# Optimization experiments

Measured on AMD Instinct MI355X. Metric: run time of the kernel, lower is better.

Reference implementation:

```python
import jax, jax.numpy as jnp
import numpy as np

B, N, D = 8, 4096, 1024
NC, NU = 8, 32            # core / universal experts (num_experts=16, occ_factor=1/4)
E = NC + NU               # 40 total experts
S = 2                     # slots per expert
HC, HU = 4 * D, D         # core hidden = 4*dim, occ hidden = 4*occ_factor*dim = dim
L2_EPS = 1e-6
LN_EPS = 1e-5


def l2norm(x):
    n = jnp.sqrt(jnp.sum(x * x, axis=-1, keepdims=True))
    return x * (1.0 / (n + L2_EPS))


def layernorm(x, g, b):
    mu = jnp.mean(x, axis=-1, keepdims=True)
    var = jnp.mean((x - mu) ** 2, axis=-1, keepdims=True)
    return (x - mu) / jnp.sqrt(var + LN_EPS) * g + b


def entmax15(z):
    # exact 1.5-entmax over last axis (sorted algorithm, Peters et al. 2019)
    z = z / 2.0
    z = z - jnp.max(z, axis=-1, keepdims=True)
    zs = -jnp.sort(-z, axis=-1)                      # descending
    K = z.shape[-1]
    k = jnp.arange(1, K + 1, dtype=z.dtype)
    mean = jnp.cumsum(zs, axis=-1) / k
    meansq = jnp.cumsum(zs * zs, axis=-1) / k
    ss = k * (meansq - mean * mean)
    delta = jnp.maximum((1.0 - ss) / k, 1e-12)
    tau = mean - jnp.sqrt(delta)
    support = jnp.sum((tau <= zs).astype(jnp.int32), axis=-1, keepdims=True)
    tau_star = jnp.take_along_axis(tau, support - 1, axis=-1)
    return jnp.maximum(z - tau_star, 0.0) ** 2


def setup_inputs() -> dict:
    key = jax.random.key(0)
    ks = jax.random.split(key, 8)
    return {
        "x": jax.random.normal(ks[0], (B, N, D), jnp.float32),
        "attn_weight": jax.random.uniform(ks[1], (B, 128), jnp.float32),
        "phi": jax.random.normal(ks[2], (E, S, D), jnp.float32) * 0.02,
        "key_gamma": jnp.ones((D,), jnp.float32),
        "key_beta": jnp.zeros((D,), jnp.float32),
        "query_gamma": jnp.ones((D,), jnp.float32),
        "query_beta": jnp.zeros((D,), jnp.float32),
        "ln_gamma": jnp.ones((D,), jnp.float32),
        "ln_beta": jnp.zeros((D,), jnp.float32),
        "scale0": jnp.asarray(0.5, jnp.float32),
        "scale1": jnp.asarray(0.5, jnp.float32),
        "core_w1": jax.random.normal(ks[3], (NC, D, HC), jnp.float32) * (D ** -0.5),
        "core_b1": jnp.zeros((NC, HC), jnp.float32),
        "core_w2": jax.random.normal(ks[4], (NC, HC, D), jnp.float32) * (HC ** -0.5),
        "core_b2": jnp.zeros((NC, D), jnp.float32),
        "occ_w1": jax.random.normal(ks[5], (NU, D, HU), jnp.float32) * (D ** -0.5),
        "occ_b1": jnp.zeros((NU, HU), jnp.float32),
        "occ_w2": jax.random.normal(ks[6], (NU, HU, D), jnp.float32) * (HU ** -0.5),
        "occ_b2": jnp.zeros((NU, D), jnp.float32),
    }


def _expert_mlp(s, w1, b1, w2, b2):
    # s: [b, e, s, d]; per-expert 2-layer MLP with exact GELU
    h = jax.nn.gelu(jnp.einsum('besd,edh->besh', s, w1) + b1[None, :, None, :], approximate=False)
    return jnp.einsum('besh,ehd->besd', h, w2) + b2[None, :, None, :]


def reference(x, attn_weight, phi, key_gamma, key_beta, query_gamma, query_beta,
              ln_gamma, ln_beta, scale0, scale1,
              core_w1, core_b1, core_w2, core_b2,
              occ_w1, occ_b1, occ_w2, occ_b2):
    # keys: OffsetScale then l2norm
    k = l2norm(x * key_gamma + key_beta)
    # queries: OffsetScale -> LayerNorm -> l2norm on phi
    q = layernorm(phi * query_gamma + query_beta, ln_gamma, ln_beta)
    q = l2norm(q)
    logits = jnp.einsum('bnd,esd->bnes', k, q)                      # [B,N,E,S]
    core_mask = (jnp.arange(E) < NC)[None, None, :, None]
    adjusted = jnp.where(core_mask, logits, jnp.asarray(-10000.0, logits.dtype))
    dispatch = jax.nn.softmax(adjusted / scale0, axis=2)            # softmax over experts
    combine = entmax15((adjusted / scale1).reshape(B, N, E * S))    # [B,N,E*S]
    slots = jnp.einsum('bnd,bnes->besd', x, dispatch)               # [B,E,S,D]
    core_out = _expert_mlp(slots[:, :NC], core_w1, core_b1, core_w2, core_b2)
    occ_out = _expert_mlp(slots[:, NC:], occ_w1, occ_b1, occ_w2, occ_b2)
    out = jnp.concatenate([core_out, occ_out], axis=1).reshape(B, E * S, D)
    return jnp.einsum('bsd,bns->bnd', out, combine)                 # [B,N,D]
```

## Files before the change

### kernel.cpp

```cpp
#include <hip/hip_runtime.h>
#include <hip/hip_bf16.h>

#define B_ 8
#define N_ 4096
#define D_ 1024

#define AS1 __attribute__((address_space(1)))
#define AS3 __attribute__((address_space(3)))
__device__ __forceinline__ void gld16(const float* g, float* l) {
    __builtin_amdgcn_global_load_lds((const AS1 void*)g, (AS3 void*)l, 16, 0, 0);
}

__global__ __launch_bounds__(64) void k_prep(
    const float* __restrict__ phi, const float* __restrict__ qg, const float* __restrict__ qb,
    const float* __restrict__ lng, const float* __restrict__ lnb,
    const float* __restrict__ kg, const float* __restrict__ kb,
    float* __restrict__ qk, float* __restrict__ cj, float* __restrict__ wbuf)
{
    int r = blockIdx.x;
    int lane = threadIdx.x;
    if (r == 16) {
        float cacc = 0.f;
#pragma unroll
        for (int c = 0; c < 16; ++c) {
            int i = c * 64 + lane;
            float g = kg[i], b = kb[i];
            wbuf[i] = g * g;
            wbuf[1024 + i] = 2.0f * g * b;
            cacc += b * b;
        }
#pragma unroll
        for (int m = 32; m; m >>= 1) cacc += __shfl_xor(cacc, m);
        if (lane == 0) wbuf[2048] = cacc;
        return;
    }
    const float* pr = phi + (size_t)r * D_;
    float v[16];
    float s1 = 0.f;
#pragma unroll
    for (int c = 0; c < 16; ++c) {
        int i = c * 64 + lane;
        v[c] = pr[i] * qg[i] + qb[i];
        s1 += v[c];
    }
#pragma unroll
    for (int m = 32; m; m >>= 1) s1 += __shfl_xor(s1, m);
    float mu = s1 * (1.0f / D_);
    float s2 = 0.f;
#pragma unroll
    for (int c = 0; c < 16; ++c) { float dd = v[c] - mu; s2 += dd * dd; }
#pragma unroll
    for (int m = 32; m; m >>= 1) s2 += __shfl_xor(s2, m);
    float var = s2 * (1.0f / D_);
    float inv = 1.0f / sqrtf(var + 1e-5f);
    float u[16];
    float s3 = 0.f;
#pragma unroll
    for (int c = 0; c < 16; ++c) {
        int i = c * 64 + lane;
        u[c] = (v[c] - mu) * inv * lng[i] + lnb[i];
        s3 += u[c] * u[c];
    }
#pragma unroll
    for (int m = 32; m; m >>= 1) s3 += __shfl_xor(s3, m);
    float rn = 1.0f / (sqrtf(s3) + 1e-6f);
    float cacc = 0.f;
#pragma unroll
    for (int c = 0; c < 16; ++c) {
        int i = c * 64 + lane;
        float qv = u[c] * rn;
        qk[(size_t)r * D_ + i] = qv * kg[i];
        cacc += qv * kb[i];
    }
#pragma unroll
    for (int m = 32; m; m >>= 1) cacc += __shfl_xor(cacc, m);
    if (lane == 0) cj[r] = cacc;
}

__global__ __launch_bounds__(256) void k_fused(
    const float* __restrict__ x, const float* __restrict__ qk,
    const float* __restrict__ wbuf, const float* __restrict__ cj,
    const float* __restrict__ s0p,
    float* __restrict__ lgbuf, float* __restrict__ spart)
{
    __shared__ float smem[18436];
    float* qs   = smem;
    float* wsd  = smem + 16384;
    float* red  = smem;
    float* sums = smem + 8704;
    float* disp = smem + 9792;

    int tid = threadIdx.x;
    int tok0 = blockIdx.x * 64;
    int wid = tid >> 6;
    int r0 = tid >> 4;
    int c4 = (tid & 15) * 4;

#pragma unroll
    for (int i = 0; i < 16; ++i)
        gld16(qk + (size_t)(i * 256 + tid) * 4, &qs[(i * 256 + wid * 64) * 4]);
#pragma unroll
    for (int i = 0; i < 2; ++i)
        gld16(wbuf + (size_t)(i * 256 + tid) * 4, &wsd[(i * 256 + wid * 64) * 4]);
    __syncthreads();

    float acc[4][17];
#pragma unroll
    for (int i = 0; i < 4; ++i)
#pragma unroll
        for (int v = 0; v < 17; ++v) acc[i][v] = 0.f;

#pragma unroll 2
    for (int dc = 0; dc < 16; ++dc) {
        float4 xv[4];
#pragma unroll
        for (int i = 0; i < 4; ++i)
            xv[i] = *(const float4*)(x + (size_t)(tok0 + i * 16 + r0) * D_ + dc * 64 + c4);
        float4 w2v = *(const float4*)(wsd + dc * 64 + c4);
        float4 w1v = *(const float4*)(wsd + 1024 + dc * 64 + c4);
#pragma unroll
        for (int i = 0; i < 4; ++i)
            acc[i][16] += (w2v.x * xv[i].x + w1v.x) * xv[i].x
                        + (w2v.y * xv[i].y + w1v.y) * xv[i].y
                        + (w2v.z * xv[i].z + w1v.z) * xv[i].z
                        + (w2v.w * xv[i].w + w1v.w) * xv[i].w;
        const float* qb = qs + dc * 64 + c4;
#pragma unroll
        for (int j = 0; j < 16; ++j) {
            float4 q4 = *(const float4*)(qb + j * 1024);
#pragma unroll
            for (int i = 0; i < 4; ++i)
                acc[i][j] += xv[i].x * q4.x + xv[i].y * q4.y
                           + xv[i].z * q4.z + xv[i].w * q4.w;
        }
    }
    __syncthreads();

#pragma unroll
    for (int half = 0; half < 2; ++half) {
#pragma unroll
        for (int u = 0; u < 2; ++u) {
            int i = half * 2 + u;
            int rr = u * 16 + r0;
#pragma unroll
            for (int v = 0; v < 17; ++v)
                red[(rr * 17 + v) * 16 + (tid & 15)] = acc[i][v];
        }
        __syncthreads();
#pragma unroll
        for (int it = 0; it < 3; ++it) {
            int idx = tid + it * 256;
            if (idx < 544) {
                const float4* p = (const float4*)(red + idx * 16);
                float4 a = p[0], b = p[1], cq = p[2], dq = p[3];
                float sum = (((a.x + a.y) + (a.z + a.w)) + ((b.x + b.y) + (b.z + b.w)))
                          + (((cq.x + cq.y) + (cq.z + cq.w)) + ((dq.x + dq.y) + (dq.z + dq.w)));
                int t = idx / 17, v = idx - t * 17;
                lgbuf[(size_t)(tok0 + half * 32 + t) * 20 + v] = sum;
                sums[(half * 32 + t) * 17 + v] = sum;
            }
        }
        __syncthreads();
    }

    if (tid < 64) {
        const float* sp = sums + tid * 17;
        float ss = sp[16] + wbuf[2048];
        float rn = 1.0f / (sqrtf(ss) + 1e-6f);
        float inv0 = 1.0f / s0p[0];
        float lg[16];
#pragma unroll
        for (int j = 0; j < 16; ++j) lg[j] = (sp[j] + cj[j]) * rn;
        float dsp[16];
#pragma unroll
        for (int sl = 0; sl < 2; ++sl) {
            float a[8], m = -1e30f;
#pragma unroll
            for (int ee = 0; ee < 8; ++ee) { a[ee] = lg[2 * ee + sl] * inv0; m = fmaxf(m, a[ee]); }
            float den = 0.f;
#pragma unroll
            for (int ee = 0; ee < 8; ++ee) { a[ee] = expf(a[ee] - m); den += a[ee]; }
            float r = 1.0f / den;
#pragma unroll
            for (int ee = 0; ee < 8; ++ee) dsp[2 * ee + sl] = a[ee] * r;
        }
#pragma unroll
        for (int q4i = 0; q4i < 4; ++q4i)
            *(float4*)(&disp[tid * 16 + q4i * 4]) =
                make_float4(dsp[q4i * 4 + 0], dsp[q4i * 4 + 1], dsp[q4i * 4 + 2], dsp[q4i * 4 + 3]);
    }
    __syncthreads();

    const float* xp = x + (size_t)tok0 * D_ + tid * 4;
    float4 acc2[16];
#pragma unroll
    for (int j = 0; j < 16; ++j) { acc2[j].x = 0.f; acc2[j].y = 0.f; acc2[j].z = 0.f; acc2[j].w = 0.f; }
#pragma unroll 8
    for (int n = 0; n < 64; ++n) {
        float4 xv = *(const float4*)(xp + (size_t)n * D_);
        const float4* q4 = (const float4*)(disp + n * 16);
        float4 s0 = q4[0], s1 = q4[1], s2 = q4[2], s3 = q4[3];
        acc2[0].x  += s0.x * xv.x; acc2[0].y  += s0.x * xv.y; acc2[0].z  += s0.x * xv.z; acc2[0].w  += s0.x * xv.w;
        acc2[1].x  += s0.y * xv.x; acc2[1].y  += s0.y * xv.y; acc2[1].z  += s0.y * xv.z; acc2[1].w  += s0.y * xv.w;
        acc2[2].x  += s0.z * xv.x; acc2[2].y  += s0.z * xv.y; acc2[2].z  += s0.z * xv.z; acc2[2].w  += s0.z * xv.w;
        acc2[3].x  += s0.w * xv.x; acc2[3].y  += s0.w * xv.y; acc2[3].z  += s0.w * xv.z; acc2[3].w  += s0.w * xv.w;
        acc2[4].x  += s1.x * xv.x; acc2[4].y  += s1.x * xv.y; acc2[4].z  += s1.x * xv.z; acc2[4].w  += s1.x * xv.w;
        acc2[5].x  += s1.y * xv.x; acc2[5].y  += s1.y * xv.y; acc2[5].z  += s1.y * xv.z; acc2[5].w  += s1.y * xv.w;
        acc2[6].x  += s1.z * xv.x; acc2[6].y  += s1.z * xv.y; acc2[6].z  += s1.z * xv.z; acc2[6].w  += s1.z * xv.w;
        acc2[7].x  += s1.w * xv.x; acc2[7].y  += s1.w * xv.y; acc2[7].z  += s1.w * xv.z; acc2[7].w  += s1.w * xv.w;
        acc2[8].x  += s2.x * xv.x; acc2[8].y  += s2.x * xv.y; acc2[8].z  += s2.x * xv.z; acc2[8].w  += s2.x * xv.w;
        acc2[9].x  += s2.y * xv.x; acc2[9].y  += s2.y * xv.y; acc2[9].z  += s2.y * xv.z; acc2[9].w  += s2.y * xv.w;
        acc2[10].x += s2.z * xv.x; acc2[10].y += s2.z * xv.y; acc2[10].z += s2.z * xv.z; acc2[10].w += s2.z * xv.w;
        acc2[11].x += s2.w * xv.x; acc2[11].y += s2.w * xv.y; acc2[11].z += s2.w * xv.z; acc2[11].w += s2.w * xv.w;
        acc2[12].x += s3.x * xv.x; acc2[12].y += s3.x * xv.y; acc2[12].z += s3.x * xv.z; acc2[12].w += s3.x * xv.w;
        acc2[13].x += s3.y * xv.x; acc2[13].y += s3.y * xv.y; acc2[13].z += s3.y * xv.z; acc2[13].w += s3.y * xv.w;
        acc2[14].x += s3.z * xv.x; acc2[14].y += s3.z * xv.y; acc2[14].z += s3.z * xv.z; acc2[14].w += s3.z * xv.w;
        acc2[15].x += s3.w * xv.x; acc2[15].y += s3.w * xv.y; acc2[15].z += s3.w * xv.z; acc2[15].w += s3.w * xv.w;
    }
    float* op = spart + ((size_t)blockIdx.x * 16) * 1024 + tid * 4;
#pragma unroll
    for (int j = 0; j < 16; ++j)
        *(float4*)(op + (size_t)j * 1024) = acc2[j];
}

__global__ __launch_bounds__(64) void k_epi(
    const float* __restrict__ lgbuf, const float* __restrict__ cj,
    const float* __restrict__ wbuf, const float* __restrict__ s1p,
    float* __restrict__ combine)
{
    int tok = blockIdx.x * 64 + threadIdx.x;
    const float* lp = lgbuf + (size_t)tok * 20;
    float s[17];
    float4 q0 = *(const float4*)(lp + 0);
    float4 q1 = *(const float4*)(lp + 4);
    float4 q2 = *(const float4*)(lp + 8);
    float4 q3 = *(const float4*)(lp + 12);
    s[0] = q0.x; s[1] = q0.y; s[2] = q0.z; s[3] = q0.w;
    s[4] = q1.x; s[5] = q1.y; s[6] = q1.z; s[7] = q1.w;
    s[8] = q2.x; s[9] = q2.y; s[10] = q2.z; s[11] = q2.w;
    s[12] = q3.x; s[13] = q3.y; s[14] = q3.z; s[15] = q3.w;
    s[16] = lp[16];

    float ss = s[16] + wbuf[2048];
    float rn = 1.0f / (sqrtf(ss) + 1e-6f);
    float inv1h = 0.5f / s1p[0];
    float lg[16];
#pragma unroll
    for (int j = 0; j < 16; ++j) lg[j] = (s[j] + cj[j]) * rn;

    float z[16], zmax = -1e30f;
#pragma unroll
    for (int j = 0; j < 16; ++j) { z[j] = lg[j] * inv1h; zmax = fmaxf(zmax, z[j]); }
#pragma unroll
    for (int j = 0; j < 16; ++j) z[j] -= zmax;
    float zsr[16];
#pragma unroll
    for (int j = 0; j < 16; ++j) zsr[j] = z[j];
#pragma unroll
    for (int rr = 0; rr < 16; ++rr) {
#pragma unroll
        for (int jj = (rr & 1); jj + 1 < 16; jj += 2) {
            float aa = zsr[jj], bb = zsr[jj + 1];
            zsr[jj] = fmaxf(aa, bb);
            zsr[jj + 1] = fminf(aa, bb);
        }
    }
    float cs = 0.f, css = 0.f, tau_star = 0.f;
#pragma unroll
    for (int kk = 1; kk <= 16; ++kk) {
        cs += zsr[kk - 1];
        css += zsr[kk - 1] * zsr[kk - 1];
        float fk = (float)kk;
        float mean = cs / fk, msq = css / fk;
        float ssv = fk * (msq - mean * mean);
        float delta = fmaxf((1.0f - ssv) / fk, 1e-12f);
        float tau = mean - sqrtf(delta);
        tau_star = (tau <= zsr[kk - 1]) ? tau : tau_star;
    }
    float4* cw = (float4*)(combine + (size_t)tok * 16);
#pragma unroll
    for (int q4i = 0; q4i < 4; ++q4i) {
        float4 cv;
        float t0 = fmaxf(z[q4i * 4 + 0] - tau_star, 0.f);
        float t1 = fmaxf(z[q4i * 4 + 1] - tau_star, 0.f);
        float t2 = fmaxf(z[q4i * 4 + 2] - tau_star, 0.f);
        float t3 = fmaxf(z[q4i * 4 + 3] - tau_star, 0.f);
        cv.x = t0 * t0; cv.y = t1 * t1; cv.z = t2 * t2; cv.w = t3 * t3;
        cw[q4i] = cv;
    }
}

__global__ __launch_bounds__(256) void k_slots_reduce(
    const float* __restrict__ spart, float* __restrict__ slotsT)
{
    int j = blockIdx.x, b = blockIdx.y;
    int tid = threadIdx.x;
    const float* p = spart + ((size_t)(b * 64) * 16 + j) * 1024 + tid * 4;
    float4 s; s.x = 0.f; s.y = 0.f; s.z = 0.f; s.w = 0.f;
#pragma unroll 8
    for (int nc = 0; nc < 64; ++nc) {
        float4 v = *(const float4*)(p + (size_t)nc * 16384);
        s.x += v.x; s.y += v.y; s.z += v.z; s.w += v.w;
    }
    int e = j >> 1, sl = j & 1;
    int t = b * 2 + sl;
    float* o = slotsT + ((size_t)e * 1024 + tid * 4) * 16 + t;
    o[0] = s.x; o[16] = s.y; o[32] = s.z; o[48] = s.w;
}

__global__ __launch_bounds__(256) void k_mlp1(
    const float* __restrict__ w1, const float* __restrict__ slotsT,
    float* __restrict__ p1)
{
    __shared__ float sm[1024];
    int cc = blockIdx.x, ks = blockIdx.y, e = blockIdx.z;
    int tid = threadIdx.x;
    int k0 = ks * 64;
    int col = cc * 1024 + tid * 4;
    ((float4*)sm)[tid] = ((const float4*)(slotsT + ((size_t)e * 1024 + k0) * 16))[tid];
    __syncthreads();

    const float* wp = w1 + (size_t)e * 1024 * 4096 + (size_t)k0 * 4096 + col;
    float4 acc[16];
#pragma unroll
    for (int t = 0; t < 16; ++t) { acc[t].x = 0.f; acc[t].y = 0.f; acc[t].z = 0.f; acc[t].w = 0.f; }
#pragma unroll 8
    for (int kk = 0; kk < 64; ++kk) {
        float4 w = *(const float4*)(wp + (size_t)kk * 4096);
        const float4* q4 = (const float4*)(sm + kk * 16);
        float4 s0 = q4[0], s1 = q4[1], s2 = q4[2], s3 = q4[3];
        acc[0].x  += s0.x * w.x; acc[0].y  += s0.x * w.y; acc[0].z  += s0.x * w.z; acc[0].w  += s0.x * w.w;
        acc[1].x  += s0.y * w.x; acc[1].y  += s0.y * w.y; acc[1].z  += s0.y * w.z; acc[1].w  += s0.y * w.w;
        acc[2].x  += s0.z * w.x; acc[2].y  += s0.z * w.y; acc[2].z  += s0.z * w.z; acc[2].w  += s0.z * w.w;
        acc[3].x  += s0.w * w.x; acc[3].y  += s0.w * w.y; acc[3].z  += s0.w * w.z; acc[3].w  += s0.w * w.w;
        acc[4].x  += s1.x * w.x; acc[4].y  += s1.x * w.y; acc[4].z  += s1.x * w.z; acc[4].w  += s1.x * w.w;
        acc[5].x  += s1.y * w.x; acc[5].y  += s1.y * w.y; acc[5].z  += s1.y * w.z; acc[5].w  += s1.y * w.w;
        acc[6].x  += s1.z * w.x; acc[6].y  += s1.z * w.y; acc[6].z  += s1.z * w.z; acc[6].w  += s1.z * w.w;
        acc[7].x  += s1.w * w.x; acc[7].y  += s1.w * w.y; acc[7].z  += s1.w * w.z; acc[7].w  += s1.w * w.w;
        acc[8].x  += s2.x * w.x; acc[8].y  += s2.x * w.y; acc[8].z  += s2.x * w.z; acc[8].w  += s2.x * w.w;
        acc[9].x  += s2.y * w.x; acc[9].y  += s2.y * w.y; acc[9].z  += s2.y * w.z; acc[9].w  += s2.y * w.w;
        acc[10].x += s2.z * w.x; acc[10].y += s2.z * w.y; acc[10].z += s2.z * w.z; acc[10].w += s2.z * w.w;
        acc[11].x += s2.w * w.x; acc[11].y += s2.w * w.y; acc[11].z += s2.w * w.z; acc[11].w += s2.w * w.w;
        acc[12].x += s3.x * w.x; acc[12].y += s3.x * w.y; acc[12].z += s3.x * w.z; acc[12].w += s3.x * w.w;
        acc[13].x += s3.y * w.x; acc[13].y += s3.y * w.y; acc[13].z += s3.y * w.z; acc[13].w += s3.y * w.w;
        acc[14].x += s3.z * w.x; acc[14].y += s3.z * w.y; acc[14].z += s3.z * w.z; acc[14].w += s3.z * w.w;
        acc[15].x += s3.w * w.x; acc[15].y += s3.w * w.y; acc[15].z += s3.w * w.z; acc[15].w += s3.w * w.w;
    }
    float av0[16], av1[16], av2[16], av3[16];
#pragma unroll
    for (int t = 0; t < 16; ++t) { av0[t] = acc[t].x; av1[t] = acc[t].y; av2[t] = acc[t].z; av3[t] = acc[t].w; }
    float* op = p1 + (((size_t)ks * 8 + e) * 4096 + col) * 16;
#pragma unroll
    for (int q = 0; q < 4; ++q) {
        *(float4*)(op + 0 * 16 + q * 4) = make_float4(av0[q*4+0], av0[q*4+1], av0[q*4+2], av0[q*4+3]);
        *(float4*)(op + 1 * 16 + q * 4) = make_float4(av1[q*4+0], av1[q*4+1], av1[q*4+2], av1[q*4+3]);
        *(float4*)(op + 2 * 16 + q * 4) = make_float4(av2[q*4+0], av2[q*4+1], av2[q*4+2], av2[q*4+3]);
        *(float4*)(op + 3 * 16 + q * 4) = make_float4(av3[q*4+0], av3[q*4+1], av3[q*4+2], av3[q*4+3]);
    }
}

__global__ __launch_bounds__(256) void k_mlp2f(
    const float* __restrict__ w2, const float* __restrict__ p1,
    const float* __restrict__ b1, float* __restrict__ p2)
{
    __shared__ float sm[1024];
    int ks = blockIdx.x, e = blockIdx.y;
    int tid = threadIdx.x;
    int k0 = ks * 64;
    int col = tid * 4;

    {
        int fidx = tid;
        const float* pp = p1 + (size_t)e * 65536 + (size_t)k0 * 16 + fidx * 4;
        float4 s; s.x = 0.f; s.y = 0.f; s.z = 0.f; s.w = 0.f;
#pragma unroll
        for (int ksp = 0; ksp < 16; ++ksp) {
            float4 v = *(const float4*)(pp + (size_t)ksp * 524288);
            s.x += v.x; s.y += v.y; s.z += v.z; s.w += v.w;
        }
        int colh = k0 + (fidx >> 2);
        float bb = b1[(size_t)e * 4096 + colh];
        s.x += bb; s.y += bb; s.z += bb; s.w += bb;
        s.x = 0.5f * s.x * (1.0f + erff(s.x * 0.70710678118654752f));
        s.y = 0.5f * s.y * (1.0f + erff(s.y * 0.70710678118654752f));
        s.z = 0.5f * s.z * (1.0f + erff(s.z * 0.70710678118654752f));
        s.w = 0.5f * s.w * (1.0f + erff(s.w * 0.70710678118654752f));
        *(float4*)(&sm[fidx * 4]) = s;
    }
    __syncthreads();

    const float* wp = w2 + (size_t)e * 4096 * 1024 + (size_t)k0 * 1024 + col;
    float4 acc[16];
#pragma unroll
    for (int t = 0; t < 16; ++t) { acc[t].x = 0.f; acc[t].y = 0.f; acc[t].z = 0.f; acc[t].w = 0.f; }
#pragma unroll 8
    for (int kk = 0; kk < 64; ++kk) {
        float4 w = *(const float4*)(wp + (size_t)kk * 1024);
        const float4* q4 = (const float4*)(sm + kk * 16);
        float4 s0 = q4[0], s1 = q4[1], s2 = q4[2], s3 = q4[3];
        acc[0].x  += s0.x * w.x; acc[0].y  += s0.x * w.y; acc[0].z  += s0.x * w.z; acc[0].w  += s0.x * w.w;
        acc[1].x  += s0.y * w.x; acc[1].y  += s0.y * w.y; acc[1].z  += s0.y * w.z; acc[1].w  += s0.y * w.w;
        acc[2].x  += s0.z * w.x; acc[2].y  += s0.z * w.y; acc[2].z  += s0.z * w.z; acc[2].w  += s0.z * w.w;
        acc[3].x  += s0.w * w.x; acc[3].y  += s0.w * w.y; acc[3].z  += s0.w * w.z; acc[3].w  += s0.w * w.w;
        acc[4].x  += s1.x * w.x; acc[4].y  += s1.x * w.y; acc[4].z  += s1.x * w.z; acc[4].w  += s1.x * w.w;
        acc[5].x  += s1.y * w.x; acc[5].y  += s1.y * w.y; acc[5].z  += s1.y * w.z; acc[5].w  += s1.y * w.w;
        acc[6].x  += s1.z * w.x; acc[6].y  += s1.z * w.y; acc[6].z  += s1.z * w.z; acc[6].w  += s1.z * w.w;
        acc[7].x  += s1.w * w.x; acc[7].y  += s1.w * w.y; acc[7].z  += s1.w * w.z; acc[7].w  += s1.w * w.w;
        acc[8].x  += s2.x * w.x; acc[8].y  += s2.x * w.y; acc[8].z  += s2.x * w.z; acc[8].w  += s2.x * w.w;
        acc[9].x  += s2.y * w.x; acc[9].y  += s2.y * w.y; acc[9].z  += s2.y * w.z; acc[9].w  += s2.y * w.w;
        acc[10].x += s2.z * w.x; acc[10].y += s2.z * w.y; acc[10].z += s2.z * w.z; acc[10].w += s2.z * w.w;
        acc[11].x += s2.w * w.x; acc[11].y += s2.w * w.y; acc[11].z += s2.w * w.z; acc[11].w += s2.w * w.w;
        acc[12].x += s3.x * w.x; acc[12].y += s3.x * w.y; acc[12].z += s3.x * w.z; acc[12].w += s3.x * w.w;
        acc[13].x += s3.y * w.x; acc[13].y += s3.y * w.y; acc[13].z += s3.y * w.z; acc[13].w += s3.y * w.w;
        acc[14].x += s3.z * w.x; acc[14].y += s3.z * w.y; acc[14].z += s3.z * w.z; acc[14].w += s3.z * w.w;
        acc[15].x += s3.w * w.x; acc[15].y += s3.w * w.y; acc[15].z += s3.w * w.z; acc[15].w += s3.w * w.w;
    }
    float av0[16], av1[16], av2[16], av3[16];
#pragma unroll
    for (int t = 0; t < 16; ++t) { av0[t] = acc[t].x; av1[t] = acc[t].y; av2[t] = acc[t].z; av3[t] = acc[t].w; }
    float* op = p2 + (((size_t)ks * 8 + e) * 1024 + col) * 16;
#pragma unroll
    for (int q = 0; q < 4; ++q) {
        *(float4*)(op + 0 * 16 + q * 4) = make_float4(av0[q*4+0], av0[q*4+1], av0[q*4+2], av0[q*4+3]);
        *(float4*)(op + 1 * 16 + q * 4) = make_float4(av1[q*4+0], av1[q*4+1], av1[q*4+2], av1[q*4+3]);
        *(float4*)(op + 2 * 16 + q * 4) = make_float4(av2[q*4+0], av2[q*4+1], av2[q*4+2], av2[q*4+3]);
        *(float4*)(op + 3 * 16 + q * 4) = make_float4(av3[q*4+0], av3[q*4+1], av3[q*4+2], av3[q*4+3]);
    }
}

__global__ __launch_bounds__(256) void k_red2(
    const float* __restrict__ p2, const float* __restrict__ b2,
    float* __restrict__ co)
{
    int idx = blockIdx.x * 256 + threadIdx.x;
    int q = idx & 3, d = (idx >> 2) & 1023, e = idx >> 12;
    const float* p = p2 + ((size_t)e * 1024 + d) * 16 + q * 4;
    float4 s; s.x = 0.f; s.y = 0.f; s.z = 0.f; s.w = 0.f;
#pragma unroll 8
    for (int ks = 0; ks < 64; ++ks) {
        float4 v = *(const float4*)(p + (size_t)ks * 131072);
        s.x += v.x; s.y += v.y; s.z += v.z; s.w += v.w;
    }
    float bb = b2[(size_t)e * 1024 + d];
    float vv[4] = { s.x + bb, s.y + bb, s.z + bb, s.w + bb };
#pragma unroll
    for (int u = 0; u < 4; ++u) {
        int t = q * 4 + u;
        int b = t >> 1, sl = t & 1;
        co[((size_t)b * 16 + e * 2 + sl) * 1024 + d] = vv[u];
    }
}

__global__ __launch_bounds__(256) void k_out(
    const float* __restrict__ co, const float* __restrict__ combine,
    float* __restrict__ out)
{
    __shared__ float sm[1024];
    int b = blockIdx.y, tile = blockIdx.x;
    int tid = threadIdx.x;
    ((float4*)sm)[tid] = ((const float4*)(combine + ((size_t)b * N_ + tile * 64) * 16))[tid];
    float4 cv[16];
#pragma unroll
    for (int j = 0; j < 16; ++j)
        cv[j] = ((const float4*)(co + ((size_t)b * 16 + j) * 1024))[tid];
    __syncthreads();
    float4* ob = (float4*)(out + ((size_t)b * N_ + tile * 64) * 1024) + tid;
#pragma unroll 2
    for (int it = 0; it < 64; ++it) {
        const float* cm = sm + it * 16;
        float4 acc; acc.x = 0.f; acc.y = 0.f; acc.z = 0.f; acc.w = 0.f;
#pragma unroll
        for (int j = 0; j < 16; ++j) {
            float wj = cm[j];
            acc.x += wj * cv[j].x; acc.y += wj * cv[j].y;
            acc.z += wj * cv[j].z; acc.w += wj * cv[j].w;
        }
        ob[(size_t)it * 256] = acc;
    }
}

extern "C" void kernel_launch(void* const* d_in, const int* in_sizes, int n_in,
                              void* d_out, int out_size, void* d_ws, size_t ws_size,
                              hipStream_t stream)
{
    const float* x   = (const float*)d_in[0];
    const float* phi = (const float*)d_in[2];
    const float* kg  = (const float*)d_in[3];
    const float* kb  = (const float*)d_in[4];
    const float* qg  = (const float*)d_in[5];
    const float* qb  = (const float*)d_in[6];
    const float* lng = (const float*)d_in[7];
    const float* lnb = (const float*)d_in[8];
    const float* s0  = (const float*)d_in[9];
    const float* s1  = (const float*)d_in[10];
    const float* w1  = (const float*)d_in[11];
    const float* b1  = (const float*)d_in[12];
    const float* w2  = (const float*)d_in[13];
    const float* b2  = (const float*)d_in[14];

    float* out = (float*)d_out;
    float* ws  = (float*)d_ws;

    float* qk       = ws;
    float* cj       = qk + 16384;
    float* wbuf     = cj + 16;
    float* combine  = wbuf + 2064;
    float* slotsT   = combine + 524288;
    float* co       = slotsT + 131072;
    float* lgbuf    = co + 131072;
    float* arenaA   = lgbuf + 655360;
    float* arenaB   = arenaA + 8388608;
    float* spart    = arenaA;
    float* p1       = arenaA;
    float* p2       = arenaB;

    k_prep        <<<dim3(17),        dim3(64),  0, stream>>>(phi, qg, qb, lng, lnb, kg, kb, qk, cj, wbuf);
    k_fused       <<<dim3(512),       dim3(256), 0, stream>>>(x, qk, wbuf, cj, s0, lgbuf, spart);
    k_epi         <<<dim3(512),       dim3(64),  0, stream>>>(lgbuf, cj, wbuf, s1, combine);
    k_slots_reduce<<<dim3(16, 8),     dim3(256), 0, stream>>>(spart, slotsT);
    k_mlp1        <<<dim3(4, 16, 8),  dim3(256), 0, stream>>>(w1, slotsT, p1);
    k_mlp2f       <<<dim3(64, 8),     dim3(256), 0, stream>>>(w2, p1, b1, p2);
    k_red2        <<<dim3(128),       dim3(256), 0, stream>>>(p2, b2, co);
    k_out         <<<dim3(64, 8),     dim3(256), 0, stream>>>(co, combine, out);
}
```

Measured before the change: 255.7 us.

## Double k_fused block to 512 threads, halving per-thread token work

The fused logits/dispatch kernel now runs 512 threads per block instead of 256. Each thread handles 2 tokens instead of 4 in the logits phase, and 32 tokens instead of 64 in the slot-accumulation phase, with the two halves summed through shared memory before writing spart. The w-vector staging in LDS is dropped and read directly from global memory, which shrinks shared memory. The aim is more parallelism and lower register pressure per thread, at the cost of an extra LDS reduction, more barriers, and less reuse of each q load across tokens.

```diff
diff --git a/kernel.cpp b/kernel.cpp
--- a/kernel.cpp
+++ b/kernel.cpp
@@ -77,15 +77,14 @@
     if (lane == 0) cj[r] = cacc;
 }
 
-__global__ __launch_bounds__(256) void k_fused(
+__global__ __launch_bounds__(512, 4) void k_fused(
     const float* __restrict__ x, const float* __restrict__ qk,
     const float* __restrict__ wbuf, const float* __restrict__ cj,
     const float* __restrict__ s0p,
     float* __restrict__ lgbuf, float* __restrict__ spart)
 {
-    __shared__ float smem[18436];
+    __shared__ float smem[16384];
     float* qs   = smem;
-    float* wsd  = smem + 16384;
     float* red  = smem;
     float* sums = smem + 8704;
     float* disp = smem + 9792;
@@ -97,41 +96,32 @@
     int c4 = (tid & 15) * 4;
 
 #pragma unroll
-    for (int i = 0; i < 16; ++i)
-        gld16(qk + (size_t)(i * 256 + tid) * 4, &qs[(i * 256 + wid * 64) * 4]);
-#pragma unroll
-    for (int i = 0; i < 2; ++i)
-        gld16(wbuf + (size_t)(i * 256 + tid) * 4, &wsd[(i * 256 + wid * 64) * 4]);
-    __syncthreads();
-
-    float acc[4][17];
-#pragma unroll
-    for (int i = 0; i < 4; ++i)
-#pragma unroll
-        for (int v = 0; v < 17; ++v) acc[i][v] = 0.f;
+    for (int i = 0; i < 8; ++i)
+        gld16(qk + (size_t)(i * 512 + tid) * 4, &qs[(i * 512 + wid * 64) * 4]);
+    __syncthreads();
+
+    float acc[2][17];
+#pragma unroll
+    for (int u = 0; u < 2; ++u)
+#pragma unroll
+        for (int v = 0; v < 17; ++v) acc[u][v] = 0.f;
 
 #pragma unroll 2
     for (int dc = 0; dc < 16; ++dc) {
-        float4 xv[4];
-#pragma unroll
-        for (int i = 0; i < 4; ++i)
-            xv[i] = *(const float4*)(x + (size_t)(tok0 + i * 16 + r0) * D_ + dc * 64 + c4);
-        float4 w2v = *(const float4*)(wsd + dc * 64 + c4);
-        float4 w1v = *(const float4*)(wsd + 1024 + dc * 64 + c4);
-#pragma unroll
-        for (int i = 0; i < 4; ++i)
-            acc[i][16] += (w2v.x * xv[i].x + w1v.x) * xv[i].x
-                        + (w2v.y * xv[i].y + w1v.y) * xv[i].y
-                        + (w2v.z * xv[i].z + w1v.z) * xv[i].z
-                        + (w2v.w * xv[i].w + w1v.w) * xv[i].w;
+        float4 xv0 = *(const float4*)(x + (size_t)(tok0 + r0) * D_ + dc * 64 + c4);
+        float4 xv1 = *(const float4*)(x + (size_t)(tok0 + 32 + r0) * D_ + dc * 64 + c4);
+        float4 w2v = *(const float4*)(wbuf + dc * 64 + c4);
+        float4 w1v = *(const float4*)(wbuf + 1024 + dc * 64 + c4);
+        acc[0][16] += (w2v.x * xv0.x + w1v.x) * xv0.x + (w2v.y * xv0.y + w1v.y) * xv0.y
+                    + (w2v.z * xv0.z + w1v.z) * xv0.z + (w2v.w * xv0.w + w1v.w) * xv0.w;
+        acc[1][16] += (w2v.x * xv1.x + w1v.x) * xv1.x + (w2v.y * xv1.y + w1v.y) * xv1.y
+                    + (w2v.z * xv1.z + w1v.z) * xv1.z + (w2v.w * xv1.w + w1v.w) * xv1.w;
         const float* qb = qs + dc * 64 + c4;
 #pragma unroll
         for (int j = 0; j < 16; ++j) {
             float4 q4 = *(const float4*)(qb + j * 1024);
-#pragma unroll
-            for (int i = 0; i < 4; ++i)
-                acc[i][j] += xv[i].x * q4.x + xv[i].y * q4.y
-                           + xv[i].z * q4.z + xv[i].w * q4.w;
+            acc[0][j] += xv0.x * q4.x + xv0.y * q4.y + xv0.z * q4.z + xv0.w * q4.w;
+            acc[1][j] += xv1.x * q4.x + xv1.y * q4.y + xv1.z * q4.z + xv1.w * q4.w;
         }
     }
     __syncthreads();
@@ -139,17 +129,12 @@
 #pragma unroll
     for (int half = 0; half < 2; ++half) {
 #pragma unroll
-        for (int u = 0; u < 2; ++u) {
-            int i = half * 2 + u;
-            int rr = u * 16 + r0;
-#pragma unroll
-            for (int v = 0; v < 17; ++v)
-                red[(rr * 17 + v) * 16 + (tid & 15)] = acc[i][v];
-        }
+        for (int v = 0; v < 17; ++v)
+            red[(r0 * 17 + v) * 16 + (tid & 15)] = acc[half][v];
         __syncthreads();
 #pragma unroll
-        for (int it = 0; it < 3; ++it) {
-            int idx = tid + it * 256;
+        for (int it = 0; it < 2; ++it) {
+            int idx = tid + it * 512;
             if (idx < 544) {
                 const float4* p = (const float4*)(red + idx * 16);
                 float4 a = p[0], b = p[1], cq = p[2], dq = p[3];
@@ -191,14 +176,16 @@
     }
     __syncthreads();
 
-    const float* xp = x + (size_t)tok0 * D_ + tid * 4;
+    int th = tid >> 8;
+    int cix = tid & 255;
+    const float* xp = x + (size_t)(tok0 + th * 32) * D_ + cix * 4;
     float4 acc2[16];
 #pragma unroll
     for (int j = 0; j < 16; ++j) { acc2[j].x = 0.f; acc2[j].y = 0.f; acc2[j].z = 0.f; acc2[j].w = 0.f; }
 #pragma unroll 8
-    for (int n = 0; n < 64; ++n) {
+    for (int n = 0; n < 32; ++n) {
         float4 xv = *(const float4*)(xp + (size_t)n * D_);
-        const float4* q4 = (const float4*)(disp + n * 16);
+        const float4* q4 = (const float4*)(disp + (th * 32 + n) * 16);
         float4 s0 = q4[0], s1 = q4[1], s2 = q4[2], s3 = q4[3];
         acc2[0].x  += s0.x * xv.x; acc2[0].y  += s0.x * xv.y; acc2[0].z  += s0.x * xv.z; acc2[0].w  += s0.x * xv.w;
         acc2[1].x  += s0.y * xv.x; acc2[1].y  += s0.y * xv.y; acc2[1].z  += s0.y * xv.z; acc2[1].w  += s0.y * xv.w;
@@ -217,10 +204,22 @@
         acc2[14].x += s3.z * xv.x; acc2[14].y += s3.z * xv.y; acc2[14].z += s3.z * xv.z; acc2[14].w += s3.z * xv.w;
         acc2[15].x += s3.w * xv.x; acc2[15].y += s3.w * xv.y; acc2[15].z += s3.w * xv.z; acc2[15].w += s3.w * xv.w;
     }
-    float* op = spart + ((size_t)blockIdx.x * 16) * 1024 + tid * 4;
-#pragma unroll
-    for (int j = 0; j < 16; ++j)
-        *(float4*)(op + (size_t)j * 1024) = acc2[j];
+    __syncthreads();
+    if (th == 1) {
+#pragma unroll
+        for (int j = 0; j < 16; ++j)
+            *(float4*)(&smem[j * 1024 + cix * 4]) = acc2[j];
+    }
+    __syncthreads();
+    if (th == 0) {
+        float* op = spart + ((size_t)blockIdx.x * 16) * 1024 + cix * 4;
+#pragma unroll
+        for (int j = 0; j < 16; ++j) {
+            float4 o = *(const float4*)(&smem[j * 1024 + cix * 4]);
+            o.x += acc2[j].x; o.y += acc2[j].y; o.z += acc2[j].z; o.w += acc2[j].w;
+            *(float4*)(op + (size_t)j * 1024) = o;
+        }
+    }
 }
 
 __global__ __launch_bounds__(64) void k_epi(
@@ -515,7 +514,7 @@
     float* p2       = arenaB;
 
     k_prep        <<<dim3(17),        dim3(64),  0, stream>>>(phi, qg, qb, lng, lnb, kg, kb, qk, cj, wbuf);
-    k_fused       <<<dim3(512),       dim3(256), 0, stream>>>(x, qk, wbuf, cj, s0, lgbuf, spart);
+    k_fused       <<<dim3(512),       dim3(512), 0, stream>>>(x, qk, wbuf, cj, s0, lgbuf, spart);
     k_epi         <<<dim3(512),       dim3(64),  0, stream>>>(lgbuf, cj, wbuf, s1, combine);
     k_slots_reduce<<<dim3(16, 8),     dim3(256), 0, stream>>>(spart, slotsT);
     k_mlp1        <<<dim3(4, 16, 8),  dim3(256), 0, stream>>>(w1, slotsT, p1);
```

Result: no change. 254.3 us (-0.6%).

## Halve LDS footprint of fused routing kernel to raise occupancy

Applied to the files above, without the earlier changes.

Shared memory in the fused logits/dispatch kernel drops from about 72KB to 32KB. The q/k matrix is now staged in two D-halves, each loaded in turn, and the small wbuf vectors are read straight from global memory instead of LDS. The per-token reduction now runs in four passes of 16 tokens instead of two passes of 32, and the dispatch loop unroll is reduced. The aim is to fit more blocks per CU, at the cost of an extra barrier and a reload stall between halves.

```diff
diff --git a/kernel.cpp b/kernel.cpp
--- a/kernel.cpp
+++ b/kernel.cpp
@@ -83,12 +83,11 @@
     const float* __restrict__ s0p,
     float* __restrict__ lgbuf, float* __restrict__ spart)
 {
-    __shared__ float smem[18436];
+    __shared__ float smem[8192];
     float* qs   = smem;
-    float* wsd  = smem + 16384;
     float* red  = smem;
-    float* sums = smem + 8704;
-    float* disp = smem + 9792;
+    float* sums = smem + 4352;
+    float* disp = smem + 5440;
 
     int tid = threadIdx.x;
     int tok0 = blockIdx.x * 64;
@@ -96,68 +95,70 @@
     int r0 = tid >> 4;
     int c4 = (tid & 15) * 4;
 
-#pragma unroll
-    for (int i = 0; i < 16; ++i)
-        gld16(qk + (size_t)(i * 256 + tid) * 4, &qs[(i * 256 + wid * 64) * 4]);
-#pragma unroll
-    for (int i = 0; i < 2; ++i)
-        gld16(wbuf + (size_t)(i * 256 + tid) * 4, &wsd[(i * 256 + wid * 64) * 4]);
+    float acc[4][17];
+#pragma unroll
+    for (int i = 0; i < 4; ++i)
+#pragma unroll
+        for (int v = 0; v < 17; ++v) acc[i][v] = 0.f;
+
+#pragma unroll 1
+    for (int dh = 0; dh < 2; ++dh) {
+        if (dh) __syncthreads();
+#pragma unroll
+        for (int i = 0; i < 8; ++i) {
+            int s = i * 256 + tid;
+            int j = s >> 7;
+            int col = (s & 127) * 4;
+            gld16(qk + (size_t)j * 1024 + dh * 512 + col,
+                  &qs[(i * 256 + wid * 64) * 4]);
+        }
+        __syncthreads();
+
+#pragma unroll 2
+        for (int dcl = 0; dcl < 8; ++dcl) {
+            int dc = dh * 8 + dcl;
+            float4 xv[4];
+#pragma unroll
+            for (int i = 0; i < 4; ++i)
+                xv[i] = *(const float4*)(x + (size_t)(tok0 + i * 16 + r0) * D_ + dc * 64 + c4);
+            float4 w2v = *(const float4*)(wbuf + dc * 64 + c4);
+            float4 w1v = *(const float4*)(wbuf + 1024 + dc * 64 + c4);
+#pragma unroll
+            for (int i = 0; i < 4; ++i)
+                acc[i][16] += (w2v.x * xv[i].x + w1v.x) * xv[i].x
+                            + (w2v.y * xv[i].y + w1v.y) * xv[i].y
+                            + (w2v.z * xv[i].z + w1v.z) * xv[i].z
+                            + (w2v.w * xv[i].w + w1v.w) * xv[i].w;
+            const float* qb = qs + dcl * 64 + c4;
+#pragma unroll
+            for (int j = 0; j < 16; ++j) {
+                float4 q4 = *(const float4*)(qb + j * 512);
+#pragma unroll
+                for (int i = 0; i < 4; ++i)
+                    acc[i][j] += xv[i].x * q4.x + xv[i].y * q4.y
+                               + xv[i].z * q4.z + xv[i].w * q4.w;
+            }
+        }
+    }
     __syncthreads();
 
-    float acc[4][17];
-#pragma unroll
-    for (int i = 0; i < 4; ++i)
-#pragma unroll
-        for (int v = 0; v < 17; ++v) acc[i][v] = 0.f;
-
-#pragma unroll 2
-    for (int dc = 0; dc < 16; ++dc) {
-        float4 xv[4];
-#pragma unroll
-        for (int i = 0; i < 4; ++i)
-            xv[i] = *(const float4*)(x + (size_t)(tok0 + i * 16 + r0) * D_ + dc * 64 + c4);
-        float4 w2v = *(const float4*)(wsd + dc * 64 + c4);
-        float4 w1v = *(const float4*)(wsd + 1024 + dc * 64 + c4);
-#pragma unroll
-        for (int i = 0; i < 4; ++i)
-            acc[i][16] += (w2v.x * xv[i].x + w1v.x) * xv[i].x
-                        + (w2v.y * xv[i].y + w1v.y) * xv[i].y
-                        + (w2v.z * xv[i].z + w1v.z) * xv[i].z
-                        + (w2v.w * xv[i].w + w1v.w) * xv[i].w;
-        const float* qb = qs + dc * 64 + c4;
-#pragma unroll
-        for (int j = 0; j < 16; ++j) {
-            float4 q4 = *(const float4*)(qb + j * 1024);
-#pragma unroll
-            for (int i = 0; i < 4; ++i)
-                acc[i][j] += xv[i].x * q4.x + xv[i].y * q4.y
-                           + xv[i].z * q4.z + xv[i].w * q4.w;
-        }
-    }
-    __syncthreads();
-
-#pragma unroll
-    for (int half = 0; half < 2; ++half) {
-#pragma unroll
-        for (int u = 0; u < 2; ++u) {
-            int i = half * 2 + u;
-            int rr = u * 16 + r0;
-#pragma unroll
-            for (int v = 0; v < 17; ++v)
-                red[(rr * 17 + v) * 16 + (tid & 15)] = acc[i][v];
-        }
+#pragma unroll 1
+    for (int p = 0; p < 4; ++p) {
+#pragma unroll
+        for (int v = 0; v < 17; ++v)
+            red[(r0 * 17 + v) * 16 + (tid & 15)] = acc[p][v];
         __syncthreads();
 #pragma unroll
-        for (int it = 0; it < 3; ++it) {
+        for (int it = 0; it < 2; ++it) {
             int idx = tid + it * 256;
-            if (idx < 544) {
-                const float4* p = (const float4*)(red + idx * 16);
-                float4 a = p[0], b = p[1], cq = p[2], dq = p[3];
+            if (idx < 272) {
+                const float4* pp = (const float4*)(red + idx * 16);
+                float4 a = pp[0], b = pp[1], cq = pp[2], dq = pp[3];
                 float sum = (((a.x + a.y) + (a.z + a.w)) + ((b.x + b.y) + (b.z + b.w)))
                           + (((cq.x + cq.y) + (cq.z + cq.w)) + ((dq.x + dq.y) + (dq.z + dq.w)));
                 int t = idx / 17, v = idx - t * 17;
-                lgbuf[(size_t)(tok0 + half * 32 + t) * 20 + v] = sum;
-                sums[(half * 32 + t) * 17 + v] = sum;
+                lgbuf[(size_t)(tok0 + p * 16 + t) * 20 + v] = sum;
+                sums[(p * 16 + t) * 17 + v] = sum;
             }
         }
         __syncthreads();
@@ -195,7 +196,7 @@
     float4 acc2[16];
 #pragma unroll
     for (int j = 0; j < 16; ++j) { acc2[j].x = 0.f; acc2[j].y = 0.f; acc2[j].z = 0.f; acc2[j].w = 0.f; }
-#pragma unroll 8
+#pragma unroll 4
     for (int n = 0; n < 64; ++n) {
         float4 xv = *(const float4*)(xp + (size_t)n * D_);
         const float4* q4 = (const float4*)(disp + n * 16);
```

After: 246.6 us. -3.6%, faster.
